# Performance work log

Hardware: AMD Instinct MI355X
Metric: run time of the kernel (lower is better)

The kernel has to match this reference:

```python
import jax, jax.numpy as jnp
import numpy as np

C_EM, H_EM, C_A = 256, 8, 32
S, R = 1024, 256
LN_EPS = 1e-5
MASK_BIAS = 1e9


def setup_inputs() -> dict:
    key = jax.random.key(0)
    ks = jax.random.split(key, 8)
    sc = 0.02
    m = jax.random.normal(ks[0], (S, R, C_EM), jnp.float32)
    # binary column mask (float mask in the original; int here so it is a constant)
    mask = (jax.random.uniform(ks[1], (S, R)) < 0.9).astype(jnp.int32)
    return {
        "m": m,
        "ln_g": jnp.ones((C_EM,), jnp.float32),
        "ln_b": jnp.zeros((C_EM,), jnp.float32),
        "w_q": jax.random.normal(ks[2], (C_EM, H_EM, C_A), jnp.float32) * sc,
        "w_k": jax.random.normal(ks[3], (C_EM, C_A), jnp.float32) * sc,
        "w_v": jax.random.normal(ks[4], (C_EM, C_A), jnp.float32) * sc,
        "w_g": jax.random.normal(ks[5], (C_EM, H_EM, C_A), jnp.float32) * sc,
        "b_g": jnp.zeros((H_EM, C_A), jnp.float32),
        "w_o": jax.random.normal(ks[6], (H_EM, C_A, C_EM), jnp.float32) * sc,
        "b_o": jnp.zeros((C_EM,), jnp.float32),
        "mask": mask,
    }


def reference(m, ln_g, ln_b, w_q, w_k, w_v, w_g, b_g, w_o, b_o, mask):
    maskf = mask.astype(m.dtype)  # [s, r]
    # LayerNorm over c_em (biased variance, eps=1e-5, torch default)
    mu = jnp.mean(m, axis=-1, keepdims=True)
    var = jnp.mean((m - mu) ** 2, axis=-1, keepdims=True)
    x = (m - mu) * jax.lax.rsqrt(var + LN_EPS) * ln_g + ln_b  # [s, r, c]
    # masked mean-pool over s -> per-column query
    q_pool = jnp.sum(x * maskf[..., None], axis=-3) / (jnp.sum(maskf, axis=-2)[..., None] + 1e-10)  # [r, c]
    Q = jnp.einsum('rc,chd->rhd', q_pool, w_q) * (1.0 / np.sqrt(C_A))  # [r, h, d]
    K = jnp.einsum('src,cd->srd', x, w_k)  # [s, r, d]
    V = jnp.einsum('src,cd->srd', x, w_v)  # [s, r, d]
    G = jax.nn.sigmoid(jnp.einsum('src,chd->srhd', x, w_g) + b_g)  # [s, r, h, d]
    bias = (maskf - 1.0) * MASK_BIAS  # [s, r]
    logits = jnp.einsum('rhd,srd->srh', Q, K) + bias[..., None]  # [s, r, h]
    A = jax.nn.softmax(logits, axis=-3)  # softmax over s
    O = jnp.einsum('srh,srd->rhd', A, V)  # [r, h, d]
    out = jnp.einsum('srhd,hdc->src', O[None, :, :, :] * G, w_o) + b_o  # [s, r, c]
    return out
```

## Files before the change

### kernel.cpp

```cpp
#include <hip/hip_runtime.h>
#include <math.h>

#define S_DIM 1024
#define R_DIM 256
#define C_DIM 256
#define SCALE 0.17677669529663687f

typedef short bf16x8 __attribute__((ext_vector_type(8)));
typedef float f32x4 __attribute__((ext_vector_type(4)));

__device__ __forceinline__ float wred(float v) {
#pragma unroll
  for (int m = 32; m >= 1; m >>= 1) v += __shfl_xor(v, m, 64);
  return v;
}

__device__ __forceinline__ short f2bf(float f) {
  union { float f; unsigned u; } v;
  v.f = f;
  unsigned r = v.u + 0x7fffu + ((v.u >> 16) & 1u);
  return (short)(r >> 16);
}

__device__ __forceinline__ float bf2f(short s) {
  union { unsigned u; float f; } v;
  v.u = ((unsigned)(unsigned short)s) << 16;
  return v.f;
}

__device__ __forceinline__ float fast_sigmoid_mul(float o, float gl) {
  return o * __builtin_amdgcn_rcpf(1.f + __expf(-gl));
}

__global__ __launch_bounds__(256)
void k0_prep(const float* __restrict__ w_g, const float* __restrict__ w_o,
             const float* __restrict__ w_k, const float* __restrict__ w_v,
             short* __restrict__ wgB, short* __restrict__ woB,
             short* __restrict__ wkvB) {
  const int id = blockIdx.x * 256 + threadIdx.x;
  if (id < 16384) {
    const int which = id >> 13;
    const int s = id & 8191;
    const int n = s & 255, g = (s >> 8) & 3, kb = s >> 10;
    const float* W = which ? w_o : w_g;
    short* Out = which ? woB : wgB;
#pragma unroll
    for (int j = 0; j < 8; ++j)
      Out[(((size_t)kb * 256 + n) * 4 + g) * 8 + j] =
          f2bf(W[(size_t)(kb * 32 + g * 8 + j) * 256 + n]);
  } else {
    const int s = id - 16384;
    const int n = s & 63, g = (s >> 6) & 3, kb = s >> 8;
    const float* W = (n < 32) ? w_k : w_v;
    const int nn = n & 31;
#pragma unroll
    for (int j = 0; j < 8; ++j)
      wkvB[(((size_t)kb * 64 + n) * 4 + g) * 8 + j] =
          f2bf(W[(size_t)(kb * 32 + g * 8 + j) * 32 + nn]);
  }
}

__global__ __launch_bounds__(256, 4)
void k1_ln_kv(const float* __restrict__ mIn, const float* __restrict__ ln_g,
              const float* __restrict__ ln_b, const short* __restrict__ wkvB,
              const int* __restrict__ mask,
              float* __restrict__ mu_ws, float* __restrict__ rs_ws,
              short* __restrict__ Kt, short* __restrict__ Vt,
              float* __restrict__ pool_ws) {
  __shared__ __align__(16) short A_lds[2048 * 8];
  __shared__ float mask_s[64];
  __shared__ float4 poolp[4][64];
  const int r  = blockIdx.y;
  const int s0 = blockIdx.x * 64;
  const int t  = threadIdx.x;

  if (t < 64) mask_s[t] = mask[(s0 + t) * R_DIM + r] ? 1.f : 0.f;

  {
    const int rw = t >> 2;
    const int q  = t & 3;
    const size_t p = (size_t)(s0 + rw) * R_DIM + r;
    const float* src = mIn + p * C_DIM + q * 64;
    float4 xv[16];
    float sum = 0.f, ssq = 0.f;
#pragma unroll
    for (int i = 0; i < 16; ++i) {
      xv[i] = *(const float4*)(src + i * 4);
      sum += xv[i].x + xv[i].y + xv[i].z + xv[i].w;
      ssq += xv[i].x * xv[i].x + xv[i].y * xv[i].y + xv[i].z * xv[i].z +
             xv[i].w * xv[i].w;
    }
    sum += __shfl_xor(sum, 1, 64); ssq += __shfl_xor(ssq, 1, 64);
    sum += __shfl_xor(sum, 2, 64); ssq += __shfl_xor(ssq, 2, 64);
    const float mu = sum * (1.f / 256.f);
    const float var = ssq * (1.f / 256.f) - mu * mu;
    const float rs = rsqrtf(var + 1e-5f);
    if (q == 0) { mu_ws[p] = mu; rs_ws[p] = rs; }

    const int gw = rw >> 4;
    const int lf0 = rw & 15;
#pragma unroll
    for (int kh = 0; kh < 2; ++kh) {
      const int kb = 2 * q + kh;
#pragma unroll
      for (int g = 0; g < 4; ++g) {
        const int lidx = kh * 32 + g * 8;
        const float4 a0 = xv[lidx >> 2], a1 = xv[(lidx >> 2) + 1];
        const float4 g0 = *(const float4*)(ln_g + kb * 32 + g * 8);
        const float4 g1 = *(const float4*)(ln_g + kb * 32 + g * 8 + 4);
        const float4 b0 = *(const float4*)(ln_b + kb * 32 + g * 8);
        const float4 b1 = *(const float4*)(ln_b + kb * 32 + g * 8 + 4);
        bf16x8 f;
        f[0] = f2bf((a0.x - mu) * rs * g0.x + b0.x);
        f[1] = f2bf((a0.y - mu) * rs * g0.y + b0.y);
        f[2] = f2bf((a0.z - mu) * rs * g0.z + b0.z);
        f[3] = f2bf((a0.w - mu) * rs * g0.w + b0.w);
        f[4] = f2bf((a1.x - mu) * rs * g1.x + b1.x);
        f[5] = f2bf((a1.y - mu) * rs * g1.y + b1.y);
        f[6] = f2bf((a1.z - mu) * rs * g1.z + b1.z);
        f[7] = f2bf((a1.w - mu) * rs * g1.w + b1.w);
        int byte = (((gw * 8 + kb) * 64 + lf0 + g * 16) << 4) ^ (((kb >> 1) & 3) << 5);
        *(bf16x8*)((char*)A_lds + byte) = f;
      }
    }
  }
  __syncthreads();

  {
    const int w = t >> 6, l = t & 63;
    const int lm = l & 15, g = l >> 4;
    f32x4 acc[4];
#pragma unroll
    for (int ni = 0; ni < 4; ++ni) acc[ni] = (f32x4){0.f, 0.f, 0.f, 0.f};
#pragma unroll
    for (int kb = 0; kb < 8; ++kb) {
      const int byte = (((w * 8 + kb) * 64 + l) << 4) ^ (((kb >> 1) & 3) << 5);
      const bf16x8 a = *(const bf16x8*)((char*)A_lds + byte);
      bf16x8 bfr[4];
#pragma unroll
      for (int ni = 0; ni < 4; ++ni)
        bfr[ni] = *(const bf16x8*)(wkvB + (((size_t)kb * 64 + lm + ni * 16) * 4 + g) * 8);
#pragma unroll
      for (int ni = 0; ni < 4; ++ni)
        acc[ni] = __builtin_amdgcn_mfma_f32_16x16x32_bf16(a, bfr[ni], acc[ni], 0, 0, 0);
    }
#pragma unroll
    for (int ni = 0; ni < 4; ++ni) {
      const int col = lm + ni * 16;
      short* Out = (col < 32) ? Kt : Vt;
      const int cc = col & 31;
#pragma unroll
      for (int reg = 0; reg < 4; ++reg) {
        const int s = s0 + w * 16 + g * 4 + reg;
        Out[((size_t)r * 1024 + s) * 32 + cc] = f2bf(acc[ni][reg]);
      }
    }
  }

  {
    const int lc = t & 63;
    const int wq = t >> 6;
    const int kb = lc >> 3, g2 = (lc >> 1) & 3, bh = (lc & 1) * 4;
    float4 ps = make_float4(0.f, 0.f, 0.f, 0.f);
    for (int i = 0; i < 16; ++i) {
      const int rloc = (i + lc) & 15;
      const int byte =
          ((((wq * 8 + kb) * 64 + rloc + g2 * 16) << 4) + bh * 2) ^ (((kb >> 1) & 3) << 5);
      const short4 xb = *(const short4*)((char*)A_lds + byte);
      const float mk = mask_s[wq * 16 + rloc];
      ps.x += mk * bf2f(xb.x);
      ps.y += mk * bf2f(xb.y);
      ps.z += mk * bf2f(xb.z);
      ps.w += mk * bf2f(xb.w);
    }
    poolp[wq][lc] = ps;
  }
  __syncthreads();
  if (t < 64) {
    const float4 a = poolp[0][t], b = poolp[1][t], c = poolp[2][t], d = poolp[3][t];
    atomicAdd(&pool_ws[r * C_DIM + t * 4 + 0], a.x + b.x + c.x + d.x);
    atomicAdd(&pool_ws[r * C_DIM + t * 4 + 1], a.y + b.y + c.y + d.y);
    atomicAdd(&pool_ws[r * C_DIM + t * 4 + 2], a.z + b.z + c.z + d.z);
    atomicAdd(&pool_ws[r * C_DIM + t * 4 + 3], a.w + b.w + c.w + d.w);
  }
}

__global__ __launch_bounds__(256, 2)
void k2_q(const float* __restrict__ pool_ws, const int* __restrict__ mask,
          const float* __restrict__ w_q, float* __restrict__ Q_ws) {
  __shared__ float qp[256];
  __shared__ float wsum[4];
  const int r = blockIdx.x, t = threadIdx.x;
  int cnt = 0;
  for (int s = t; s < S_DIM; s += 256) cnt += mask[s * R_DIM + r];
  float cf = wred((float)cnt);
  if ((t & 63) == 0) wsum[t >> 6] = cf;
  __syncthreads();
  const float denom = wsum[0] + wsum[1] + wsum[2] + wsum[3] + 1e-10f;
  qp[t] = pool_ws[r * C_DIM + t] / denom;
  __syncthreads();
  float acc = 0.f;
  for (int c = 0; c < 256; ++c) acc += qp[c] * w_q[c * 256 + t];
  Q_ws[r * 256 + t] = acc * SCALE;
}

__global__ __launch_bounds__(256, 4)
void k3eb(const short* __restrict__ Kt, const short* __restrict__ Vt,
          const float* __restrict__ Q_ws, const int* __restrict__ mask,
          float* __restrict__ Npart, float* __restrict__ D_ws) {
  __shared__ float q[256];
  __shared__ float A_s[8 * 256];
  __shared__ __align__(16) short V_s[256 * 32];
  const int ch = blockIdx.x, r = blockIdx.y;
  const int t = threadIdx.x;
  const int sb = ch * 256;

  q[t] = Q_ws[r * 256 + t];
  {
    const short* vp = Vt + ((size_t)r * 1024 + sb) * 32;
#pragma unroll
    for (int i = 0; i < 4; ++i) {
      const int u = i * 256 + t;
      *(bf16x8*)(V_s + u * 8) = *(const bf16x8*)(vp + u * 8);
    }
  }
  const int s = sb + t;
  const short* kp = Kt + ((size_t)r * 1024 + s) * 32;
  bf16x8 kr[4];
#pragma unroll
  for (int i = 0; i < 4; ++i) kr[i] = *(const bf16x8*)(kp + i * 8);
  const int mk = mask[s * R_DIM + r];
  __syncthreads();

  float kf[32];
#pragma unroll
  for (int i = 0; i < 4; ++i)
#pragma unroll
    for (int j = 0; j < 8; ++j) kf[i * 8 + j] = bf2f(kr[i][j]);
#pragma unroll
  for (int h = 0; h < 8; ++h) {
    float a = 0.f;
#pragma unroll
    for (int d = 0; d < 32; ++d) a += q[h * 32 + d] * kf[d];
    A_s[h * 256 + t] = mk ? __expf(a) : 0.f;
  }
  __syncthreads();

  const int h = t >> 5, d = t & 31;
  const float* ap = A_s + h * 256;
  float o = 0.f;
  for (int s4 = 0; s4 < 256; s4 += 4) {
    const float4 a4 = *(const float4*)(ap + s4);
    o += a4.x * bf2f(V_s[(s4 + 0) * 32 + d]);
    o += a4.y * bf2f(V_s[(s4 + 1) * 32 + d]);
    o += a4.z * bf2f(V_s[(s4 + 2) * 32 + d]);
    o += a4.w * bf2f(V_s[(s4 + 3) * 32 + d]);
  }
  Npart[(size_t)ch * 65536 + r * 256 + t] = o;
  float ds = 0.f;
  for (int s1 = d; s1 < 256; s1 += 32) ds += ap[s1];
#pragma unroll
  for (int mkk = 16; mkk >= 1; mkk >>= 1) ds += __shfl_xor(ds, mkk, 64);
  if (d == 0) atomicAdd(&D_ws[r * 8 + h], ds);
}

__global__ __launch_bounds__(256)
void k3c_norm(const float* __restrict__ Npart, const float* __restrict__ D_ws,
              float* __restrict__ O_ws) {
  const int r = blockIdx.x, t = threadIdx.x;
  const int idx = r * 256 + t;
  const float n = Npart[idx] + Npart[65536 + idx] + Npart[131072 + idx] +
                  Npart[196608 + idx];
  O_ws[idx] = n / (D_ws[r * 8 + (t >> 5)] + 1e-30f);
}

__global__ __launch_bounds__(256, 4)
void k4_mfma(const float* __restrict__ mIn, const float* __restrict__ ln_g,
             const float* __restrict__ ln_b, const float* __restrict__ mu_ws,
             const float* __restrict__ rs_ws, const short* __restrict__ wgB,
             const float* __restrict__ b_g, const float* __restrict__ O_ws,
             const short* __restrict__ woB, const float* __restrict__ b_o,
             float* __restrict__ out) {
  __shared__ __align__(16) short A_lds[2048 * 8];
  const int t = threadIdx.x;
  const int p0 = blockIdx.x * 64;
  const int r0 = p0 & 255;
  const int l = t & 63;
  const int w = t >> 6;
  const int lm = l & 15;
  const int g = l >> 4;

  {
    const int row = w * 16 + lm;
    const size_t p = (size_t)(p0 + row);
    const float mu = mu_ws[p], rs = rs_ws[p];
    const float* mrow = mIn + p * 256 + g * 8;
    const float* gp = ln_g + g * 8;
    const float* bp = ln_b + g * 8;
#pragma unroll
    for (int kb = 0; kb < 8; ++kb) {
      const float4 m0 = *(const float4*)(mrow + kb * 32);
      const float4 m1 = *(const float4*)(mrow + kb * 32 + 4);
      const float4 g0 = *(const float4*)(gp + kb * 32);
      const float4 g1 = *(const float4*)(gp + kb * 32 + 4);
      const float4 b0 = *(const float4*)(bp + kb * 32);
      const float4 b1 = *(const float4*)(bp + kb * 32 + 4);
      bf16x8 xf;
      xf[0] = f2bf((m0.x - mu) * rs * g0.x + b0.x);
      xf[1] = f2bf((m0.y - mu) * rs * g0.y + b0.y);
      xf[2] = f2bf((m0.z - mu) * rs * g0.z + b0.z);
      xf[3] = f2bf((m0.w - mu) * rs * g0.w + b0.w);
      xf[4] = f2bf((m1.x - mu) * rs * g1.x + b1.x);
      xf[5] = f2bf((m1.y - mu) * rs * g1.y + b1.y);
      xf[6] = f2bf((m1.z - mu) * rs * g1.z + b1.z);
      xf[7] = f2bf((m1.w - mu) * rs * g1.w + b1.w);
      *(bf16x8*)(A_lds + ((w * 8 + kb) * 64 + l) * 8) = xf;
    }
  }
  __syncthreads();

  const int col = w * 64 + lm;
  f32x4 acc[4][4];

#pragma unroll
  for (int ni = 0; ni < 4; ++ni) {
    const float bg = b_g[col + ni * 16];
#pragma unroll
    for (int mi = 0; mi < 4; ++mi) acc[mi][ni] = (f32x4){bg, bg, bg, bg};
  }
#pragma unroll
  for (int kb = 0; kb < 8; ++kb) {
    bf16x8 a[4], bb[4];
#pragma unroll
    for (int mi = 0; mi < 4; ++mi)
      a[mi] = *(const bf16x8*)(A_lds + ((mi * 8 + kb) * 64 + l) * 8);
#pragma unroll
    for (int ni = 0; ni < 4; ++ni)
      bb[ni] = *(const bf16x8*)(wgB + (((size_t)kb * 256 + col + ni * 16) * 4 + g) * 8);
#pragma unroll
    for (int mi = 0; mi < 4; ++mi)
#pragma unroll
      for (int ni = 0; ni < 4; ++ni)
        acc[mi][ni] = __builtin_amdgcn_mfma_f32_16x16x32_bf16(a[mi], bb[ni], acc[mi][ni], 0, 0, 0);
  }
  __syncthreads();

#pragma unroll
  for (int mi = 0; mi < 4; ++mi) {
#pragma unroll
    for (int ni = 0; ni < 4; ++ni) {
      const int c2 = col + ni * 16;
      const int kb2 = c2 >> 5, g2 = (c2 >> 3) & 3, b2 = c2 & 7;
#pragma unroll
      for (int reg = 0; reg < 4; ++reg) {
        const int row = mi * 16 + g * 4 + reg;
        const float o = O_ws[(r0 + row) * 256 + c2];
        const float tv = fast_sigmoid_mul(o, acc[mi][ni][reg]);
        const int u = (mi * 8 + kb2) * 64 + (g * 4 + reg) + g2 * 16;
        const int byte = ((u << 4) ^ (((u >> 4) & 3) << 4)) + b2 * 2;
        *(short*)((char*)A_lds + byte) = f2bf(tv);
      }
    }
  }
  __syncthreads();

#pragma unroll
  for (int ni = 0; ni < 4; ++ni) {
    const float bo = b_o[col + ni * 16];
#pragma unroll
    for (int mi = 0; mi < 4; ++mi) acc[mi][ni] = (f32x4){bo, bo, bo, bo};
  }
#pragma unroll
  for (int kb = 0; kb < 8; ++kb) {
    bf16x8 a[4], bb[4];
#pragma unroll
    for (int mi = 0; mi < 4; ++mi) {
      const int u = (mi * 8 + kb) * 64 + l;
      const int byte = (u << 4) ^ (g << 4);
      a[mi] = *(const bf16x8*)((char*)A_lds + byte);
    }
#pragma unroll
    for (int ni = 0; ni < 4; ++ni)
      bb[ni] = *(const bf16x8*)(woB + (((size_t)kb * 256 + col + ni * 16) * 4 + g) * 8);
#pragma unroll
    for (int mi = 0; mi < 4; ++mi)
#pragma unroll
      for (int ni = 0; ni < 4; ++ni)
        acc[mi][ni] = __builtin_amdgcn_mfma_f32_16x16x32_bf16(a[mi], bb[ni], acc[mi][ni], 0, 0, 0);
  }

#pragma unroll
  for (int mi = 0; mi < 4; ++mi)
#pragma unroll
    for (int ni = 0; ni < 4; ++ni)
#pragma unroll
      for (int reg = 0; reg < 4; ++reg) {
        const int row = mi * 16 + g * 4 + reg;
        out[(size_t)(p0 + row) * 256 + col + ni * 16] = acc[mi][ni][reg];
      }
}

extern "C" void kernel_launch(void* const* d_in, const int* in_sizes, int n_in,
                              void* d_out, int out_size, void* d_ws, size_t ws_size,
                              hipStream_t stream) {
  const float* mIn  = (const float*)d_in[0];
  const float* ln_g = (const float*)d_in[1];
  const float* ln_b = (const float*)d_in[2];
  const float* w_q  = (const float*)d_in[3];
  const float* w_k  = (const float*)d_in[4];
  const float* w_v  = (const float*)d_in[5];
  const float* w_g  = (const float*)d_in[6];
  const float* b_g  = (const float*)d_in[7];
  const float* w_o  = (const float*)d_in[8];
  const float* b_o  = (const float*)d_in[9];
  const int*   mask = (const int*)d_in[10];
  float* outp = (float*)d_out;

  float* ws = (float*)d_ws;
  const size_t NP = (size_t)S_DIM * R_DIM;
  float* mu_ws   = ws;
  float* rs_ws   = mu_ws + NP;
  short* Kt      = (short*)(rs_ws + NP);
  short* Vt      = Kt + (size_t)256 * 1024 * 32;
  float* pool_ws = (float*)(Vt + (size_t)256 * 1024 * 32);
  float* D_ws    = pool_ws + 65536;
  float* Q_ws    = D_ws + 2048;
  float* Npart   = Q_ws + 65536;
  float* O_ws    = Npart + 262144;
  short* wgB     = (short*)(O_ws + 65536);
  short* woB     = wgB + 65536;
  short* wkvB    = woB + 65536;

  hipMemsetAsync(pool_ws, 0, (65536 + 2048) * sizeof(float), stream);

  k0_prep<<<72, 256, 0, stream>>>(w_g, w_o, w_k, w_v, wgB, woB, wkvB);
  k1_ln_kv<<<dim3(S_DIM / 64, R_DIM), 256, 0, stream>>>(
      mIn, ln_g, ln_b, wkvB, mask, mu_ws, rs_ws, Kt, Vt, pool_ws);
  k2_q<<<R_DIM, 256, 0, stream>>>(pool_ws, mask, w_q, Q_ws);
  k3eb<<<dim3(4, R_DIM), 256, 0, stream>>>(Kt, Vt, Q_ws, mask, Npart, D_ws);
  k3c_norm<<<R_DIM, 256, 0, stream>>>(Npart, D_ws, O_ws);
  k4_mfma<<<dim3(S_DIM * R_DIM / 64), 256, 0, stream>>>(
      mIn, ln_g, ln_b, mu_ws, rs_ws, wgB, b_g, O_ws, woB, b_o, outp);
}
```

Baseline: 352.5 us.

## Stash normalized bf16 activations in k1 and reuse them in the output kernel

k1 now writes its swizzled bf16 LayerNorm tile from LDS out to a global stash. A new k4_stash kernel loads that tile directly instead of re-reading the fp32 input and recomputing LayerNorm, then runs the gate and output GEMMs. This is meant to halve the bytes k4 reads from the 256MB input (32KB bf16 tile instead of 64KB fp32 per block) and to skip the normalization math. In exchange k1 writes an extra 128MB to workspace. The stash path only runs when the workspace is large enough; otherwise it falls back to the old kernel.

```diff
diff --git a/kernel.cpp b/kernel.cpp
--- a/kernel.cpp
+++ b/kernel.cpp
@@ -66,7 +66,7 @@
               const int* __restrict__ mask,
               float* __restrict__ mu_ws, float* __restrict__ rs_ws,
               short* __restrict__ Kt, short* __restrict__ Vt,
-              float* __restrict__ pool_ws) {
+              float* __restrict__ pool_ws, char* __restrict__ xstash) {
   __shared__ __align__(16) short A_lds[2048 * 8];
   __shared__ float mask_s[64];
   __shared__ float4 poolp[4][64];
@@ -126,6 +126,15 @@
   }
   __syncthreads();
 
+  if (xstash) {
+    char* dst = xstash + (((size_t)blockIdx.x * 256 + r) << 15);
+#pragma unroll
+    for (int i = 0; i < 8; ++i) {
+      const int u = i * 256 + t;
+      *(bf16x8*)(dst + u * 16) = *(const bf16x8*)((const char*)A_lds + u * 16);
+    }
+  }
+
   {
     const int w = t >> 6, l = t & 63;
     const int lm = l & 15, g = l >> 4;
@@ -272,6 +281,112 @@
   const float n = Npart[idx] + Npart[65536 + idx] + Npart[131072 + idx] +
                   Npart[196608 + idx];
   O_ws[idx] = n / (D_ws[r * 8 + (t >> 5)] + 1e-30f);
+}
+
+__global__ __launch_bounds__(256, 4)
+void k4_stash(const char* __restrict__ xstash, const short* __restrict__ wgB,
+              const float* __restrict__ b_g, const float* __restrict__ O_ws,
+              const short* __restrict__ woB, const float* __restrict__ b_o,
+              float* __restrict__ out) {
+  __shared__ __align__(16) short A_lds[2048 * 8];
+  const int t = threadIdx.x;
+  const int s0 = blockIdx.x * 64;
+  const int r  = blockIdx.y;
+  const int l = t & 63, w = t >> 6, lm = l & 15, g = l >> 4;
+  const char* base = xstash + (((size_t)blockIdx.x * 256 + r) << 15);
+
+  bf16x8 stg[8];
+#pragma unroll
+  for (int i = 0; i < 8; ++i) stg[i] = *(const bf16x8*)(base + (i * 256 + t) * 16);
+#pragma unroll
+  for (int i = 0; i < 8; ++i)
+    *(bf16x8*)((char*)A_lds + (i * 256 + t) * 16) = stg[i];
+  __syncthreads();
+
+  const int col = w * 64 + lm;
+  float o4[4], bg4[4], bo4[4];
+#pragma unroll
+  for (int ni = 0; ni < 4; ++ni) {
+    o4[ni]  = O_ws[r * 256 + col + ni * 16];
+    bg4[ni] = b_g[col + ni * 16];
+    bo4[ni] = b_o[col + ni * 16];
+  }
+
+  f32x4 acc[4][4];
+#pragma unroll
+  for (int ni = 0; ni < 4; ++ni)
+#pragma unroll
+    for (int mi = 0; mi < 4; ++mi)
+      acc[mi][ni] = (f32x4){bg4[ni], bg4[ni], bg4[ni], bg4[ni]};
+
+#pragma unroll
+  for (int kb = 0; kb < 8; ++kb) {
+    const int swz = ((kb >> 1) & 3) << 5;
+    bf16x8 a[4], bb[4];
+#pragma unroll
+    for (int mi = 0; mi < 4; ++mi)
+      a[mi] = *(const bf16x8*)((char*)A_lds + ((((mi * 8 + kb) * 64 + l) << 4) ^ swz));
+#pragma unroll
+    for (int ni = 0; ni < 4; ++ni)
+      bb[ni] = *(const bf16x8*)(wgB + (((size_t)kb * 256 + col + ni * 16) * 4 + g) * 8);
+#pragma unroll
+    for (int mi = 0; mi < 4; ++mi)
+#pragma unroll
+      for (int ni = 0; ni < 4; ++ni)
+        acc[mi][ni] = __builtin_amdgcn_mfma_f32_16x16x32_bf16(a[mi], bb[ni], acc[mi][ni], 0, 0, 0);
+  }
+  __syncthreads();
+
+#pragma unroll
+  for (int mi = 0; mi < 4; ++mi) {
+#pragma unroll
+    for (int ni = 0; ni < 4; ++ni) {
+      const int c2 = col + ni * 16;
+      const int kb2 = c2 >> 5, g2 = (c2 >> 3) & 3, b2 = c2 & 7;
+#pragma unroll
+      for (int reg = 0; reg < 4; ++reg) {
+        const float tv = fast_sigmoid_mul(o4[ni], acc[mi][ni][reg]);
+        const int u = (mi * 8 + kb2) * 64 + (g * 4 + reg) + g2 * 16;
+        const int byte = ((u << 4) ^ (((u >> 4) & 3) << 4)) + b2 * 2;
+        *(short*)((char*)A_lds + byte) = f2bf(tv);
+      }
+    }
+  }
+  __syncthreads();
+
+#pragma unroll
+  for (int ni = 0; ni < 4; ++ni)
+#pragma unroll
+    for (int mi = 0; mi < 4; ++mi)
+      acc[mi][ni] = (f32x4){bo4[ni], bo4[ni], bo4[ni], bo4[ni]};
+#pragma unroll
+  for (int kb = 0; kb < 8; ++kb) {
+    bf16x8 a[4], bb[4];
+#pragma unroll
+    for (int mi = 0; mi < 4; ++mi) {
+      const int u = (mi * 8 + kb) * 64 + l;
+      a[mi] = *(const bf16x8*)((char*)A_lds + ((u << 4) ^ (g << 4)));
+    }
+#pragma unroll
+    for (int ni = 0; ni < 4; ++ni)
+      bb[ni] = *(const bf16x8*)(woB + (((size_t)kb * 256 + col + ni * 16) * 4 + g) * 8);
+#pragma unroll
+    for (int mi = 0; mi < 4; ++mi)
+#pragma unroll
+      for (int ni = 0; ni < 4; ++ni)
+        acc[mi][ni] = __builtin_amdgcn_mfma_f32_16x16x32_bf16(a[mi], bb[ni], acc[mi][ni], 0, 0, 0);
+  }
+
+#pragma unroll
+  for (int mi = 0; mi < 4; ++mi)
+#pragma unroll
+    for (int ni = 0; ni < 4; ++ni)
+#pragma unroll
+      for (int reg = 0; reg < 4; ++reg) {
+        const int row = mi * 16 + g * 4 + reg;
+        out[((size_t)((s0 + row) * R_DIM + r)) * 256 + col + ni * 16] =
+            acc[mi][ni][reg];
+      }
 }
 
 __global__ __launch_bounds__(256, 4)
@@ -420,9 +535,7 @@
   const size_t NP = (size_t)S_DIM * R_DIM;
   float* mu_ws   = ws;
   float* rs_ws   = mu_ws + NP;
-  short* Kt      = (short*)(rs_ws + NP);
-  short* Vt      = Kt + (size_t)256 * 1024 * 32;
-  float* pool_ws = (float*)(Vt + (size_t)256 * 1024 * 32);
+  float* pool_ws = rs_ws + NP;
   float* D_ws    = pool_ws + 65536;
   float* Q_ws    = D_ws + 2048;
   float* Npart   = Q_ws + 65536;
@@ -430,15 +543,26 @@
   short* wgB     = (short*)(O_ws + 65536);
   short* woB     = wgB + 65536;
   short* wkvB    = woB + 65536;
+  short* Kt      = wkvB + 16384;
+  short* Vt      = Kt + (size_t)256 * 1024 * 32;
+  char*  xstash  = (char*)(Vt + (size_t)256 * 1024 * 32);
+  const size_t need = (size_t)((char*)xstash - (char*)d_ws) + ((size_t)4096 << 15);
+  const bool use_stash = (ws_size >= need);
 
   hipMemsetAsync(pool_ws, 0, (65536 + 2048) * sizeof(float), stream);
 
   k0_prep<<<72, 256, 0, stream>>>(w_g, w_o, w_k, w_v, wgB, woB, wkvB);
   k1_ln_kv<<<dim3(S_DIM / 64, R_DIM), 256, 0, stream>>>(
-      mIn, ln_g, ln_b, wkvB, mask, mu_ws, rs_ws, Kt, Vt, pool_ws);
+      mIn, ln_g, ln_b, wkvB, mask, mu_ws, rs_ws, Kt, Vt, pool_ws,
+      use_stash ? xstash : (char*)nullptr);
   k2_q<<<R_DIM, 256, 0, stream>>>(pool_ws, mask, w_q, Q_ws);
   k3eb<<<dim3(4, R_DIM), 256, 0, stream>>>(Kt, Vt, Q_ws, mask, Npart, D_ws);
   k3c_norm<<<R_DIM, 256, 0, stream>>>(Npart, D_ws, O_ws);
-  k4_mfma<<<dim3(S_DIM * R_DIM / 64), 256, 0, stream>>>(
-      mIn, ln_g, ln_b, mu_ws, rs_ws, wgB, b_g, O_ws, woB, b_o, outp);
-}
+  if (use_stash) {
+    k4_stash<<<dim3(S_DIM / 64, R_DIM), 256, 0, stream>>>(
+        xstash, wgB, b_g, O_ws, woB, b_o, outp);
+  } else {
+    k4_mfma<<<dim3(S_DIM * R_DIM / 64), 256, 0, stream>>>(
+        mIn, ln_g, ln_b, mu_ws, rs_ws, wgB, b_g, O_ws, woB, b_o, outp);
+  }
+}
```

After: 373.5 us. 1.06x slower.
